# Kernel tuning notes

Measured on AMD Instinct MI355X. Metric: run time of the kernel, lower is better.

The kernel has to match this reference:

```python
import jax, jax.numpy as jnp
import numpy as np

N = 100000   # num_nodes
E = 1600000  # num_edges
IN, HID, OUT = 128, 128, 64
BN_EPS = 1e-5


def setup_inputs() -> dict:
    key = jax.random.key(0)
    ks = jax.random.split(key, 8)
    x = jax.random.normal(ks[0], (N, IN), jnp.float32)
    edge_index = jax.random.randint(ks[1], (2, E), 0, N)
    edge_weight = jax.random.uniform(ks[2], (E,), jnp.float32)
    W1 = jax.random.normal(ks[3], (IN, HID), jnp.float32) / np.sqrt(IN)
    b1 = jnp.zeros((HID,), jnp.float32)
    gamma = jnp.ones((HID,), jnp.float32)
    beta = jnp.zeros((HID,), jnp.float32)
    W2 = jax.random.normal(ks[4], (HID, OUT), jnp.float32) / np.sqrt(HID)
    b2 = jnp.zeros((OUT,), jnp.float32)
    return {"x": x, "edge_index": edge_index, "edge_weight": edge_weight,
            "W1": W1, "b1": b1, "gamma": gamma, "beta": beta, "W2": W2, "b2": b2}


def _add_self_loops(edge_index, edge_weight, n):
    loops = jnp.arange(n, dtype=edge_index.dtype)
    row = jnp.concatenate([edge_index[0], loops])
    col = jnp.concatenate([edge_index[1], loops])
    ew = jnp.concatenate([edge_weight, jnp.ones((n,), edge_weight.dtype)])
    return row, col, ew


def _gcn_conv(x, row, col, ew, W, b, n):
    h = x @ W                                           # [n, out]
    deg = jax.ops.segment_sum(ew, col, num_segments=n)  # in-degree (incl. self-loops)
    dinv = jnp.where(deg > 0, jax.lax.rsqrt(jnp.where(deg > 0, deg, 1.0)), 0.0)
    norm = dinv[row] * ew * dinv[col]                   # [E+n]
    msg = h[row] * norm[:, None]                        # gather + scale
    out = jax.ops.segment_sum(msg, col, num_segments=n)  # scatter-add at targets
    return out + b


def reference(x, edge_index, edge_weight, W1, b1, gamma, beta, W2, b2):
    n = x.shape[0]
    row, col, ew = _add_self_loops(edge_index, edge_weight, n)
    h = _gcn_conv(x, row, col, ew, W1, b1, n)
    # BatchNorm1d over nodes (training-mode batch stats, biased variance)
    mu = h.mean(axis=0)
    var = ((h - mu) ** 2).mean(axis=0)
    h = (h - mu) * jax.lax.rsqrt(var + BN_EPS) * gamma + beta
    h = jax.nn.relu(h)
    # dropout is identity at inference
    h = _gcn_conv(h, row, col, ew, W2, b2, n)
    return jax.nn.log_softmax(h, axis=1)  # out_feats > 1 branch
```

## Files before the change

kernel.cpp:

```cpp
#include <hip/hip_runtime.h>
#include <math.h>


typedef unsigned int   uint;
typedef unsigned short ushort;
typedef __bf16 bf16x8 __attribute__((ext_vector_type(8)));
typedef float  f32x4  __attribute__((ext_vector_type(4)));

#define EPB  4096
#define BSH  9

union U16 { uint4 u; bf16x8 b; };

__device__ __forceinline__ void atomAddF(float* p, float v) {
    __hip_atomic_fetch_add(p, v, __ATOMIC_RELAXED, __HIP_MEMORY_SCOPE_AGENT);
}

__device__ __forceinline__ ushort f2bf(float f) {
    uint u = __float_as_uint(f);
    u += 0x7FFFu + ((u >> 16) & 1u);
    return (ushort)(u >> 16);
}
__device__ __forceinline__ float bf2f(ushort h) {
    return __uint_as_float(((uint)h) << 16);
}
__device__ __forceinline__ uint pack2(float f0, float f1) {
    return (uint)f2bf(f0) | ((uint)f2bf(f1) << 16);
}
__device__ __forceinline__ void fma8(float* acc, uint4 v, float w) {
    acc[0] = fmaf(bf2f((ushort)(v.x)),       w, acc[0]);
    acc[1] = fmaf(bf2f((ushort)(v.x >> 16)), w, acc[1]);
    acc[2] = fmaf(bf2f((ushort)(v.y)),       w, acc[2]);
    acc[3] = fmaf(bf2f((ushort)(v.y >> 16)), w, acc[3]);
    acc[4] = fmaf(bf2f((ushort)(v.z)),       w, acc[4]);
    acc[5] = fmaf(bf2f((ushort)(v.z >> 16)), w, acc[5]);
    acc[6] = fmaf(bf2f((ushort)(v.w)),       w, acc[6]);
    acc[7] = fmaf(bf2f((ushort)(v.w >> 16)), w, acc[7]);
}

__global__ __launch_bounds__(256)
void k_p1(const int* __restrict__ col, int* __restrict__ ghist,
          int e, int PB) {
    __shared__ int lh[256];
    lh[threadIdx.x] = 0;
    __syncthreads();
    int base = blockIdx.x * EPB;
    int end  = base + EPB; if (end > e) end = e;
    for (int j = base + threadIdx.x; j < end; j += 256)
        atomicAdd(&lh[col[j] >> BSH], 1);
    __syncthreads();
    ghist[threadIdx.x * PB + blockIdx.x] = lh[threadIdx.x];
}

__global__ __launch_bounds__(256)
void k_scanA(const int* __restrict__ v, int* __restrict__ bsum, int tot) {
    __shared__ int ls[256];
    int base = blockIdx.x * 1024 + threadIdx.x * 4;
    int s = 0;
#pragma unroll
    for (int k = 0; k < 4; ++k) { int i = base + k; if (i < tot) s += v[i]; }
    ls[threadIdx.x] = s;
    __syncthreads();
    for (int d = 128; d > 0; d >>= 1) {
        if (threadIdx.x < d) ls[threadIdx.x] += ls[threadIdx.x + d];
        __syncthreads();
    }
    if (threadIdx.x == 0) bsum[blockIdx.x] = ls[0];
}

__global__ __launch_bounds__(1024)
void k_scanB(int* __restrict__ bsum, float* __restrict__ bn, int nblk) {
    __shared__ int ls[1024];
    int t = threadIdx.x;
    if (t < 256) bn[t] = 0.0f;
    int v = (t < nblk) ? bsum[t] : 0;
    ls[t] = v;
    __syncthreads();
    for (int d = 1; d < 1024; d <<= 1) {
        int mine = ls[t];
        int up   = (t >= d) ? ls[t - d] : 0;
        __syncthreads();
        ls[t] = mine + up;
        __syncthreads();
    }
    if (t < nblk) bsum[t] = ls[t] - v;
}

__global__ __launch_bounds__(256)
void k_scanC(const int* __restrict__ v, const int* __restrict__ bsum,
             int* __restrict__ gout, int tot) {
    __shared__ int ls[256];
    int base = blockIdx.x * 1024 + threadIdx.x * 4;
    int w[4];
#pragma unroll
    for (int k = 0; k < 4; ++k) { int i = base + k; w[k] = (i < tot) ? v[i] : 0; }
    int t = w[0] + w[1] + w[2] + w[3];
    ls[threadIdx.x] = t;
    __syncthreads();
    for (int d = 1; d < 256; d <<= 1) {
        int mine = ls[threadIdx.x];
        int up   = (threadIdx.x >= d) ? ls[threadIdx.x - d] : 0;
        __syncthreads();
        ls[threadIdx.x] = mine + up;
        __syncthreads();
    }
    int off = bsum[blockIdx.x] + ls[threadIdx.x] - t;
    int pf = 0;
#pragma unroll
    for (int k = 0; k < 4; ++k) {
        int i = base + k;
        if (i < tot) gout[i] = off + pf;
        pf += w[k];
    }
}

__global__ __launch_bounds__(256)
void k_p3(const int* __restrict__ row, const int* __restrict__ col,
          const float* __restrict__ ew, const int* __restrict__ goff,
          int2* __restrict__ ebuf, int e, int PB) {
    __shared__ int cur[256];
    cur[threadIdx.x] = 0;
    __syncthreads();
    int blk  = blockIdx.x;
    int base = blk * EPB;
    int end  = base + EPB; if (end > e) end = e;
    for (int j = base + threadIdx.x; j < end; j += 256) {
        int c = col[j];
        int b = c >> BSH;
        int r = atomicAdd(&cur[b], 1);
        int pos = goff[b * PB + blk] + r;
        ebuf[pos] = make_int2(row[j] | ((c & ((1 << BSH) - 1)) << 17),
                              __float_as_int(ew[j]));
    }
}

__global__ __launch_bounds__(512)
void k_p4(const int* __restrict__ goff, const int2* __restrict__ ebuf,
          int2* __restrict__ csr, int* __restrict__ ptr,
          float* __restrict__ dinv, int n, int e, int PB, int NB) {
    __shared__ int   cnt[512];
    __shared__ float fs[512];
    __shared__ int   cur2[512];
    __shared__ int   sc[512];
    int tid = threadIdx.x;
    int b   = blockIdx.x;
    int bstart = goff[b * PB];
    int bend   = (b == NB - 1) ? e : goff[(b + 1) * PB];

    cnt[tid] = 0; fs[tid] = 0.f; cur2[tid] = 0;
    __syncthreads();

    for (int j = bstart + tid; j < bend; j += 512) {
        int2 eb = ebuf[j];
        int c = (eb.x >> 17) & 511;
        atomicAdd(&cnt[c], 1);
        atomicAdd(&fs[c], __int_as_float(eb.y));
    }
    __syncthreads();

    int v = cnt[tid];
    sc[tid] = v;
    __syncthreads();
    for (int d = 1; d < 512; d <<= 1) {
        int mine = sc[tid];
        int up   = (tid >= d) ? sc[tid - d] : 0;
        __syncthreads();
        sc[tid] = mine + up;
        __syncthreads();
    }
    int excl = sc[tid] - v;

    int node = (b << BSH) + tid;
    if (node < n) {
        ptr[node]  = bstart + excl;
        dinv[node] = rsqrtf(1.0f + fs[tid]);
    }
    cnt[tid] = excl;
    __syncthreads();

    for (int j = bstart + tid; j < bend; j += 512) {
        int2 eb = ebuf[j];
        int c = (eb.x >> 17) & 511;
        int r = atomicAdd(&cur2[c], 1);
        csr[bstart + cnt[c] + r] = make_int2(eb.x & 0x1FFFF, eb.y);
    }
    if (b == 0 && tid == 0) ptr[n] = e;
}

__global__ void k_wfrag(const float* __restrict__ W, uint4* __restrict__ Wf, int M) {
    int t = blockIdx.x * 256 + threadIdx.x;
    if (t >= M * 16) return;
    int l  = t & 63;
    int ks = (t >> 6) & 3;
    int nt = t >> 8;
    int kbase = ks * 32 + (l >> 4) * 8;
    int colj  = nt * 16 + (l & 15);
    float v[8];
#pragma unroll
    for (int j = 0; j < 8; ++j) v[j] = W[(kbase + j) * M + colj];
    uint4 o;
    o.x = pack2(v[0], v[1]);
    o.y = pack2(v[2], v[3]);
    o.z = pack2(v[4], v[5]);
    o.w = pack2(v[6], v[7]);
    Wf[t] = o;
}

template<int M, bool BN>
__global__ __launch_bounds__(256)
void k_mfma(const void* __restrict__ Xv, const uint4* __restrict__ Wf,
            const float* __restrict__ scale, const float* __restrict__ shift,
            ushort* __restrict__ H, int n)
{
    constexpr int NT = M / 16;
    const int l = threadIdx.x & 63;
    const int w = threadIdx.x >> 6;
    const int rowbase = blockIdx.x * 64 + w * 16;
    const int arow = rowbase + (l & 15);
    const bool rv = arow < n;
    const int koff = (l >> 4) * 8;

    f32x4 acc[NT];
#pragma unroll
    for (int t = 0; t < NT; ++t) acc[t] = (f32x4){0.f, 0.f, 0.f, 0.f};

#pragma unroll
    for (int ks = 0; ks < 4; ++ks) {
        U16 ua;
        if (BN) {
            const ushort* xr = (const ushort*)Xv + (size_t)arow * 128 + koff;
            U16 xa; xa.u = make_uint4(0, 0, 0, 0);
            if (rv) xa.u = *(const uint4*)(xr + ks * 32);
            int k0 = ks * 32 + koff;
            float4 sc0 = *(const float4*)(scale + k0);
            float4 sc1 = *(const float4*)(scale + k0 + 4);
            float4 sh0 = *(const float4*)(shift + k0);
            float4 sh1 = *(const float4*)(shift + k0 + 4);
            float a[8];
            a[0] = fmaxf(0.f, fmaf(bf2f((ushort)(xa.u.x)),       sc0.x, sh0.x));
            a[1] = fmaxf(0.f, fmaf(bf2f((ushort)(xa.u.x >> 16)), sc0.y, sh0.y));
            a[2] = fmaxf(0.f, fmaf(bf2f((ushort)(xa.u.y)),       sc0.z, sh0.z));
            a[3] = fmaxf(0.f, fmaf(bf2f((ushort)(xa.u.y >> 16)), sc0.w, sh0.w));
            a[4] = fmaxf(0.f, fmaf(bf2f((ushort)(xa.u.z)),       sc1.x, sh1.x));
            a[5] = fmaxf(0.f, fmaf(bf2f((ushort)(xa.u.z >> 16)), sc1.y, sh1.y));
            a[6] = fmaxf(0.f, fmaf(bf2f((ushort)(xa.u.w)),       sc1.z, sh1.z));
            a[7] = fmaxf(0.f, fmaf(bf2f((ushort)(xa.u.w >> 16)), sc1.w, sh1.w));
            ua.u.x = pack2(a[0], a[1]);
            ua.u.y = pack2(a[2], a[3]);
            ua.u.z = pack2(a[4], a[5]);
            ua.u.w = pack2(a[6], a[7]);
        } else {
            const float* xr = (const float*)Xv + (size_t)arow * 128 + koff;
            float4 a0 = make_float4(0.f, 0.f, 0.f, 0.f);
            float4 a1 = a0;
            if (rv) {
                a0 = *(const float4*)(xr + ks * 32);
                a1 = *(const float4*)(xr + ks * 32 + 4);
            }
            ua.u.x = pack2(a0.x, a0.y);
            ua.u.y = pack2(a0.z, a0.w);
            ua.u.z = pack2(a1.x, a1.y);
            ua.u.w = pack2(a1.z, a1.w);
        }
#pragma unroll
        for (int nt = 0; nt < NT; ++nt) {
            U16 ub;
            ub.u = Wf[(nt * 4 + ks) * 64 + l];
            acc[nt] = __builtin_amdgcn_mfma_f32_16x16x32_bf16(ua.b, ub.b, acc[nt], 0, 0, 0);
        }
    }

    __shared__ __align__(16) ushort lds[4][16][M + 8];
#pragma unroll
    for (int nt = 0; nt < NT; ++nt)
#pragma unroll
        for (int r = 0; r < 4; ++r)
            lds[w][(l >> 4) * 4 + r][nt * 16 + (l & 15)] = f2bf(acc[nt][r]);
    __syncthreads();

    constexpr int LPR = M / 8;
    constexpr int RPP = 64 / LPR;
#pragma unroll
    for (int it = 0; it < 16 / RPP; ++it) {
        int rl = it * RPP + (l / LPR);
        int gr = rowbase + rl;
        if (gr < n)
            *(uint4*)(H + (size_t)gr * M + (l % LPR) * 8) =
                *(const uint4*)&lds[w][rl][(l % LPR) * 8];
    }
}

__global__ __launch_bounds__(256)
void k_gather1(const int* __restrict__ ptr, const int2* __restrict__ csr,
               const ushort* __restrict__ h, const float* __restrict__ dinv,
               const float* __restrict__ bias, ushort* __restrict__ out, int n)
{
    int lane = threadIdx.x & 7;
    int node = (blockIdx.x * 256 + threadIdx.x) >> 3;
    if (node >= n) return;
    int p0 = ptr[node], p1 = ptr[node + 1];
    float di = dinv[node];
    float s  = di * di;

    const ushort* hrow = h + (size_t)node * 128 + lane * 16;
    U16 h0, h1v; h0.u = *(const uint4*)hrow; h1v.u = *(const uint4*)(hrow + 8);
    float acc[16];
    {
        const float* bp = bias + lane * 16;
#pragma unroll
        for (int k = 0; k < 16; ++k) acc[k] = bp[k];
        fma8(acc,     h0.u,  s);
        fma8(acc + 8, h1v.u, s);
    }

#pragma unroll 4
    for (int j = p0; j < p1; ++j) {
        int2 pr = csr[j];
        float w = __int_as_float(pr.y) * di * dinv[pr.x];
        const ushort* sr = h + (size_t)pr.x * 128 + lane * 16;
        U16 v0, v1; v0.u = *(const uint4*)sr; v1.u = *(const uint4*)(sr + 8);
        fma8(acc,     v0.u, w);
        fma8(acc + 8, v1.u, w);
    }

    U16 o0, o1;
    o0.u.x = pack2(acc[0],  acc[1]);
    o0.u.y = pack2(acc[2],  acc[3]);
    o0.u.z = pack2(acc[4],  acc[5]);
    o0.u.w = pack2(acc[6],  acc[7]);
    o1.u.x = pack2(acc[8],  acc[9]);
    o1.u.y = pack2(acc[10], acc[11]);
    o1.u.z = pack2(acc[12], acc[13]);
    o1.u.w = pack2(acc[14], acc[15]);
    ushort* orow = out + (size_t)node * 128 + lane * 16;
    *(uint4*)(orow)     = o0.u;
    *(uint4*)(orow + 8) = o1.u;
}

__global__ __launch_bounds__(256)
void k_gather2(const int* __restrict__ ptr, const int2* __restrict__ csr,
               const ushort* __restrict__ h, const float* __restrict__ dinv,
               const float* __restrict__ bias, float* __restrict__ out, int n)
{
    int lane = threadIdx.x & 7;
    int node = (blockIdx.x * 256 + threadIdx.x) >> 3;
    if (node >= n) return;
    int p0 = ptr[node], p1 = ptr[node + 1];
    float di = dinv[node];
    float s  = di * di;

    U16 hv; hv.u = *(const uint4*)(h + (size_t)node * 64 + lane * 8);
    float acc[8];
    {
        const float* bp = bias + lane * 8;
#pragma unroll
        for (int k = 0; k < 8; ++k) acc[k] = bp[k];
        fma8(acc, hv.u, s);
    }

#pragma unroll 4
    for (int j = p0; j < p1; ++j) {
        int2 pr = csr[j];
        float w = __int_as_float(pr.y) * di * dinv[pr.x];
        U16 v; v.u = *(const uint4*)(h + (size_t)pr.x * 64 + lane * 8);
        fma8(acc, v.u, w);
    }

    float m = acc[0];
#pragma unroll
    for (int k = 1; k < 8; ++k) m = fmaxf(m, acc[k]);
#pragma unroll
    for (int off = 1; off < 8; off <<= 1) m = fmaxf(m, __shfl_xor(m, off, 64));
    float sum = 0.f;
#pragma unroll
    for (int k = 0; k < 8; ++k) sum += expf(acc[k] - m);
#pragma unroll
    for (int off = 1; off < 8; off <<= 1) sum += __shfl_xor(sum, off, 64);
    float lse = m + logf(sum);

    float* orow = out + (size_t)node * 64 + lane * 8;
    *(float4*)(orow)     = make_float4(acc[0] - lse, acc[1] - lse, acc[2] - lse, acc[3] - lse);
    *(float4*)(orow + 4) = make_float4(acc[4] - lse, acc[5] - lse, acc[6] - lse, acc[7] - lse);
}

__global__ __launch_bounds__(256)
void k_bn_stats(const ushort* __restrict__ a, float* __restrict__ sums,
                float* __restrict__ sumsq, int n)
{
    int fp = threadIdx.x & 63;
    int rg = threadIdx.x >> 6;
    float s0 = 0.f, q0 = 0.f, s1 = 0.f, q1 = 0.f;
    for (int r = blockIdx.x * 4 + rg; r < n; r += gridDim.x * 4) {
        uint v = *(const uint*)(a + (size_t)r * 128 + fp * 2);
        float x0 = bf2f((ushort)v), x1 = bf2f((ushort)(v >> 16));
        s0 += x0; q0 += x0 * x0;
        s1 += x1; q1 += x1 * x1;
    }
    __shared__ float l0[256], l1[256], l2[256], l3[256];
    l0[threadIdx.x] = s0; l1[threadIdx.x] = q0;
    l2[threadIdx.x] = s1; l3[threadIdx.x] = q1;
    __syncthreads();
    if (rg == 0) {
        float S0 = l0[fp] + l0[fp + 64] + l0[fp + 128] + l0[fp + 192];
        float Q0 = l1[fp] + l1[fp + 64] + l1[fp + 128] + l1[fp + 192];
        float S1 = l2[fp] + l2[fp + 64] + l2[fp + 128] + l2[fp + 192];
        float Q1 = l3[fp] + l3[fp + 64] + l3[fp + 128] + l3[fp + 192];
        atomAddF(&sums[fp * 2],      S0);
        atomAddF(&sumsq[fp * 2],     Q0);
        atomAddF(&sums[fp * 2 + 1],  S1);
        atomAddF(&sumsq[fp * 2 + 1], Q1);
    }
}

__global__ void k_bn_final(const float* __restrict__ bn, const float* __restrict__ gamma,
                           const float* __restrict__ beta, float* __restrict__ scale,
                           float* __restrict__ shift, int n)
{
    int f = threadIdx.x;
    if (f < 128) {
        float inv_n = 1.0f / (float)n;
        float mu  = bn[f] * inv_n;
        float var = bn[128 + f] * inv_n - mu * mu;
        float rstd = rsqrtf(var + 1e-5f);
        float sc = gamma[f] * rstd;
        scale[f] = sc;
        shift[f] = beta[f] - mu * sc;
    }
}

extern "C" void kernel_launch(void* const* d_in, const int* in_sizes, int n_in,
                              void* d_out, int out_size, void* d_ws, size_t ws_size,
                              hipStream_t stream)
{
    const float* x     = (const float*)d_in[0];
    const int*   ei    = (const int*)  d_in[1];
    const float* ew    = (const float*)d_in[2];
    const float* W1    = (const float*)d_in[3];
    const float* b1    = (const float*)d_in[4];
    const float* gamma = (const float*)d_in[5];
    const float* beta  = (const float*)d_in[6];
    const float* W2    = (const float*)d_in[7];
    const float* b2    = (const float*)d_in[8];

    const int n = in_sizes[0] / 128;
    const int e = in_sizes[2];
    const int* row = ei;
    const int* col = ei + e;

    const int PB  = (e + EPB - 1) / EPB;
    const int NB  = (n + (1 << BSH) - 1) >> BSH;
    const int tot = NB * PB;

    float* ws    = (float*)d_ws;
    size_t off   = 0;
    float* dinv  = ws + off; off += n;
    ushort* h1   = (ushort*)(ws + off); off += (size_t)n * 64;
    ushort* agg1 = (ushort*)(ws + off); off += (size_t)n * 64;
    float* bn    = ws + off; off += 256;
    float* scale = ws + off; off += 128;
    float* shift = ws + off; off += 128;
    int*   ptr   = (int*)(ws + off); off += (size_t)(n + 1);
    int*   bsum  = (int*)(ws + off); off += 1024;
    int*   ghist = (int*)(ws + off); off += (size_t)PB * 256;
    int*   goff  = (int*)(ws + off); off += (size_t)(tot + 1);
    off = (off + 3) & ~(size_t)3;
    uint4* w1f   = (uint4*)(ws + off); off += 8192;
    uint4* w2f   = (uint4*)(ws + off); off += 4096;
    int2*  ebuf  = (int2*)(ws + off); off += (size_t)e * 2;
    int2*  csr   = (int2*)(ws + off); off += (size_t)e * 2;
    ushort* h2   = h1;
    float* outp  = (float*)d_out;

    const int nb_opn = (n + 31) / 32;
    const int nb_mf  = (n + 63) / 64;
    const int nblk_scan = (tot + 1023) / 1024;

    k_wfrag<<<8, 256, 0, stream>>>(W1, w1f, 128);
    k_wfrag<<<4, 256, 0, stream>>>(W2, w2f, 64);

    k_p1<<<PB, 256, 0, stream>>>(col, ghist, e, PB);
    k_scanA<<<nblk_scan, 256, 0, stream>>>(ghist, bsum, tot);
    k_scanB<<<1, 1024, 0, stream>>>(bsum, bn, nblk_scan);
    k_scanC<<<nblk_scan, 256, 0, stream>>>(ghist, bsum, goff, tot);
    k_p3<<<PB, 256, 0, stream>>>(row, col, ew, goff, ebuf, e, PB);
    k_p4<<<NB, 512, 0, stream>>>(goff, ebuf, csr, ptr, dinv, n, e, PB, NB);

    k_mfma<128, false><<<nb_mf, 256, 0, stream>>>(x, w1f, nullptr, nullptr, h1, n);
    k_gather1<<<nb_opn, 256, 0, stream>>>(ptr, csr, h1, dinv, b1, agg1, n);

    k_bn_stats<<<256, 256, 0, stream>>>(agg1, bn, bn + 128, n);
    k_bn_final<<<1, 128, 0, stream>>>(bn, gamma, beta, scale, shift, n);

    k_mfma<64, true><<<nb_mf, 256, 0, stream>>>(agg1, w2f, scale, shift, h2, n);
    k_gather2<<<nb_opn, 256, 0, stream>>>(ptr, csr, h2, dinv, b2, outp, n);
}
```

Baseline: 241.4 us.

## Precompute normalized edge weights in CSR and batch gathers eight edges at a time

Splits the CSR build into two kernels so the full dinv array exists before edges are written. Each CSR entry then stores the final symmetric-normalized weight, which removes the per-edge dinv lookup from both gather kernels. The gathers now load eight edges' indices and feature rows before accumulating, giving more memory-level parallelism. Layer 1 uses 16 lanes per node with 8 features each, doubling thread count. The cost is an extra kernel launch, a second pass over ebuf, and a random dinv read during the CSR build.

```diff
diff --git a/kernel.cpp b/kernel.cpp
--- a/kernel.cpp
+++ b/kernel.cpp
@@ -135,19 +135,18 @@
 }
 
 __global__ __launch_bounds__(512)
-void k_p4(const int* __restrict__ goff, const int2* __restrict__ ebuf,
-          int2* __restrict__ csr, int* __restrict__ ptr,
-          float* __restrict__ dinv, int n, int e, int PB, int NB) {
+void k_p4a(const int* __restrict__ goff, const int2* __restrict__ ebuf,
+           int* __restrict__ ptr, float* __restrict__ dinv,
+           int n, int e, int PB, int NB) {
     __shared__ int   cnt[512];
     __shared__ float fs[512];
-    __shared__ int   cur2[512];
     __shared__ int   sc[512];
     int tid = threadIdx.x;
     int b   = blockIdx.x;
     int bstart = goff[b * PB];
     int bend   = (b == NB - 1) ? e : goff[(b + 1) * PB];
 
-    cnt[tid] = 0; fs[tid] = 0.f; cur2[tid] = 0;
+    cnt[tid] = 0; fs[tid] = 0.f;
     __syncthreads();
 
     for (int j = bstart + tid; j < bend; j += 512) {
@@ -175,16 +174,33 @@
         ptr[node]  = bstart + excl;
         dinv[node] = rsqrtf(1.0f + fs[tid]);
     }
-    cnt[tid] = excl;
+    if (b == 0 && tid == 0) ptr[n] = e;
+}
+
+__global__ __launch_bounds__(512)
+void k_p4b(const int* __restrict__ goff, const int2* __restrict__ ebuf,
+           const int* __restrict__ ptr, const float* __restrict__ dinv,
+           int2* __restrict__ csr, int n, int e, int PB, int NB) {
+    __shared__ int   cur[512];
+    __shared__ float dl[512];
+    int tid = threadIdx.x;
+    int b   = blockIdx.x;
+    int bstart = goff[b * PB];
+    int bend   = (b == NB - 1) ? e : goff[(b + 1) * PB];
+
+    cur[tid] = 0;
+    int node = (b << BSH) + tid;
+    dl[tid] = (node < n) ? dinv[node] : 0.f;
     __syncthreads();
 
     for (int j = bstart + tid; j < bend; j += 512) {
         int2 eb = ebuf[j];
-        int c = (eb.x >> 17) & 511;
-        int r = atomicAdd(&cur2[c], 1);
-        csr[bstart + cnt[c] + r] = make_int2(eb.x & 0x1FFFF, eb.y);
-    }
-    if (b == 0 && tid == 0) ptr[n] = e;
+        int c   = (eb.x >> 17) & 511;
+        int src = eb.x & 0x1FFFF;
+        int r = atomicAdd(&cur[c], 1);
+        float w = __int_as_float(eb.y) * dinv[src] * dl[c];
+        csr[ptr[(b << BSH) + c] + r] = make_int2(src, __float_as_int(w));
+    }
 }
 
 __global__ void k_wfrag(const float* __restrict__ W, uint4* __restrict__ Wf, int M) {
@@ -295,46 +311,48 @@
                const ushort* __restrict__ h, const float* __restrict__ dinv,
                const float* __restrict__ bias, ushort* __restrict__ out, int n)
 {
-    int lane = threadIdx.x & 7;
-    int node = (blockIdx.x * 256 + threadIdx.x) >> 3;
+    int lane = threadIdx.x & 15;
+    int node = (blockIdx.x * 256 + threadIdx.x) >> 4;
     if (node >= n) return;
     int p0 = ptr[node], p1 = ptr[node + 1];
     float di = dinv[node];
     float s  = di * di;
 
-    const ushort* hrow = h + (size_t)node * 128 + lane * 16;
-    U16 h0, h1v; h0.u = *(const uint4*)hrow; h1v.u = *(const uint4*)(hrow + 8);
-    float acc[16];
+    U16 hv; hv.u = *(const uint4*)(h + (size_t)node * 128 + lane * 8);
+    float acc[8];
     {
-        const float* bp = bias + lane * 16;
-#pragma unroll
-        for (int k = 0; k < 16; ++k) acc[k] = bp[k];
-        fma8(acc,     h0.u,  s);
-        fma8(acc + 8, h1v.u, s);
-    }
-
-#pragma unroll 4
-    for (int j = p0; j < p1; ++j) {
+        const float* bp = bias + lane * 8;
+#pragma unroll
+        for (int k = 0; k < 8; ++k) acc[k] = bp[k];
+        fma8(acc, hv.u, s);
+    }
+
+    int j = p0;
+    int jend8 = p0 + ((p1 - p0) & ~7);
+    for (; j < jend8; j += 8) {
+        int2 pr[8];
+#pragma unroll
+        for (int k = 0; k < 8; ++k) pr[k] = csr[j + k];
+        uint4 v[8];
+#pragma unroll
+        for (int k = 0; k < 8; ++k)
+            v[k] = *(const uint4*)(h + (size_t)pr[k].x * 128 + lane * 8);
+#pragma unroll
+        for (int k = 0; k < 8; ++k)
+            fma8(acc, v[k], __int_as_float(pr[k].y));
+    }
+    for (; j < p1; ++j) {
         int2 pr = csr[j];
-        float w = __int_as_float(pr.y) * di * dinv[pr.x];
-        const ushort* sr = h + (size_t)pr.x * 128 + lane * 16;
-        U16 v0, v1; v0.u = *(const uint4*)sr; v1.u = *(const uint4*)(sr + 8);
-        fma8(acc,     v0.u, w);
-        fma8(acc + 8, v1.u, w);
-    }
-
-    U16 o0, o1;
-    o0.u.x = pack2(acc[0],  acc[1]);
-    o0.u.y = pack2(acc[2],  acc[3]);
-    o0.u.z = pack2(acc[4],  acc[5]);
-    o0.u.w = pack2(acc[6],  acc[7]);
-    o1.u.x = pack2(acc[8],  acc[9]);
-    o1.u.y = pack2(acc[10], acc[11]);
-    o1.u.z = pack2(acc[12], acc[13]);
-    o1.u.w = pack2(acc[14], acc[15]);
-    ushort* orow = out + (size_t)node * 128 + lane * 16;
-    *(uint4*)(orow)     = o0.u;
-    *(uint4*)(orow + 8) = o1.u;
+        uint4 v = *(const uint4*)(h + (size_t)pr.x * 128 + lane * 8);
+        fma8(acc, v, __int_as_float(pr.y));
+    }
+
+    U16 o;
+    o.u.x = pack2(acc[0], acc[1]);
+    o.u.y = pack2(acc[2], acc[3]);
+    o.u.z = pack2(acc[4], acc[5]);
+    o.u.w = pack2(acc[6], acc[7]);
+    *(uint4*)(out + (size_t)node * 128 + lane * 8) = o.u;
 }
 
 __global__ __launch_bounds__(256)
@@ -358,12 +376,24 @@
         fma8(acc, hv.u, s);
     }
 
-#pragma unroll 4
-    for (int j = p0; j < p1; ++j) {
+    int j = p0;
+    int jend8 = p0 + ((p1 - p0) & ~7);
+    for (; j < jend8; j += 8) {
+        int2 pr[8];
+#pragma unroll
+        for (int k = 0; k < 8; ++k) pr[k] = csr[j + k];
+        uint4 v[8];
+#pragma unroll
+        for (int k = 0; k < 8; ++k)
+            v[k] = *(const uint4*)(h + (size_t)pr[k].x * 64 + lane * 8);
+#pragma unroll
+        for (int k = 0; k < 8; ++k)
+            fma8(acc, v[k], __int_as_float(pr[k].y));
+    }
+    for (; j < p1; ++j) {
         int2 pr = csr[j];
-        float w = __int_as_float(pr.y) * di * dinv[pr.x];
-        U16 v; v.u = *(const uint4*)(h + (size_t)pr.x * 64 + lane * 8);
-        fma8(acc, v.u, w);
+        uint4 v = *(const uint4*)(h + (size_t)pr.x * 64 + lane * 8);
+        fma8(acc, v, __int_as_float(pr.y));
     }
 
     float m = acc[0];
@@ -471,6 +501,7 @@
     ushort* h2   = h1;
     float* outp  = (float*)d_out;
 
+    const int nb_qpn = (n + 15) / 16;
     const int nb_opn = (n + 31) / 32;
     const int nb_mf  = (n + 63) / 64;
     const int nblk_scan = (tot + 1023) / 1024;
@@ -483,10 +514,11 @@
     k_scanB<<<1, 1024, 0, stream>>>(bsum, bn, nblk_scan);
     k_scanC<<<nblk_scan, 256, 0, stream>>>(ghist, bsum, goff, tot);
     k_p3<<<PB, 256, 0, stream>>>(row, col, ew, goff, ebuf, e, PB);
-    k_p4<<<NB, 512, 0, stream>>>(goff, ebuf, csr, ptr, dinv, n, e, PB, NB);
+    k_p4a<<<NB, 512, 0, stream>>>(goff, ebuf, ptr, dinv, n, e, PB, NB);
+    k_p4b<<<NB, 512, 0, stream>>>(goff, ebuf, ptr, dinv, csr, n, e, PB, NB);
 
     k_mfma<128, false><<<nb_mf, 256, 0, stream>>>(x, w1f, nullptr, nullptr, h1, n);
-    k_gather1<<<nb_opn, 256, 0, stream>>>(ptr, csr, h1, dinv, b1, agg1, n);
+    k_gather1<<<nb_qpn, 256, 0, stream>>>(ptr, csr, h1, dinv, b1, agg1, n);
 
     k_bn_stats<<<256, 256, 0, stream>>>(agg1, bn, bn + 128, n);
     k_bn_final<<<1, 128, 0, stream>>>(bn, gamma, beta, scale, shift, n);
```

Result: slower. 256.8 us (+6.3%).
